# Optimization experiments

Measured on AMD Instinct MI355X. Metric: run time of the kernel, lower is better.

The kernel has to match this reference:

```python
import jax, jax.numpy as jnp
import numpy as np
import math

B, L, D, N = 8, 4096, 1024, 16

def setup_inputs() -> dict:
    key = jax.random.key(0)
    k1, k2, k3, k4, k5, k6 = jax.random.split(key, 6)
    return {
        "x": jax.random.normal(k1, (B, L, D), dtype=jnp.float32),
        "delta": jax.random.normal(k2, (D, N, 1), dtype=jnp.float32),
        "alpha": jax.random.normal(k3, (D, N, 1), dtype=jnp.float32),
        "beta": jax.random.normal(k4, (D, N, 1), dtype=jnp.float32),
        "gamma": jax.random.normal(k5, (D, N), dtype=jnp.float32),
        "omega": jax.random.normal(k6, (D,), dtype=jnp.float32),
    }

def reference(x, delta, alpha, beta, gamma, omega):
    # x: (B, L, D). Unidirectional EMA, no state, no padding mask.
    b, l, d = x.shape
    n_state = gamma.shape[-1]
    scale = math.sqrt(1.0 / n_state)

    residual = x * omega  # (B, L, D)
    xt = jnp.swapaxes(x, -1, -2)  # (B, D, L)

    # EMA coefficients
    p = jax.nn.sigmoid(delta)          # (D, N, 1)
    a = jax.nn.sigmoid(alpha)          # (D, N, 1)
    q = 1.0 - p * a                    # (D, N, 1)

    # Vandermonde kernel: k[d, t] = sum_n p*beta*q^t * gamma*scale
    t = jnp.arange(l, dtype=x.dtype)   # (L,)
    vander = t[None, None, :] * jnp.log(q)          # (D, N, L)
    kernel = p * beta * jnp.exp(vander)             # (D, N, L)
    k = jnp.einsum('dnl,dn->dl', kernel, gamma * scale)  # (D, L)

    # FFT long convolution with zero-padding to 2L (linear conv)
    n_fft = 2 * l
    k_f = jnp.fft.rfft(k, n=n_fft)                  # (D, L+1) complex
    x_f = jnp.fft.rfft(xt, n=n_fft)                 # (B, D, L+1) complex
    out = jnp.fft.irfft(x_f * k_f, n=n_fft)[..., :l]  # (B, D, L)

    return jnp.swapaxes(out, -1, -2) + residual     # (B, L, D)
```

## Files before the change

### kernel.cpp

```cpp
#include <hip/hip_runtime.h>


#define BB 8
#define LL 4096
#define DD 1024
#define NN 16
#define UF 8
#define NB 512

__device__ __forceinline__ float sigmoid_precise(float v) {
    return 1.0f / (1.0f + expf(-v));
}

__device__ __forceinline__ void sc_store(float* p, float v) {
    asm volatile("global_store_dword %0, %1, off sc0 sc1"
                 :: "v"(p), "v"(v) : "memory");
}
__device__ __forceinline__ int sc_load_i(const int* p) {
    int v;
    asm volatile("global_load_dword %0, %1, off sc0 sc1\n\t"
                 "s_waitcnt vmcnt(0)"
                 : "=v"(v) : "v"(p) : "memory");
    return v;
}
__device__ __forceinline__ void sc_load4(const float* p0, const float* p1,
                                         const float* p2, const float* p3,
                                         float& o0, float& o1, float& o2, float& o3) {
    asm volatile(
        "global_load_dword %0, %4, off sc0 sc1\n\t"
        "global_load_dword %1, %5, off sc0 sc1\n\t"
        "global_load_dword %2, %6, off sc0 sc1\n\t"
        "global_load_dword %3, %7, off sc0 sc1\n\t"
        "s_waitcnt vmcnt(0)"
        : "=&v"(o0), "=&v"(o1), "=&v"(o2), "=&v"(o3)
        : "v"(p0), "v"(p1), "v"(p2), "v"(p3)
        : "memory");
}
__device__ __forceinline__ void sc_load8s(const float* p, size_t stride, float* o) {
    const float* a0 = p;
    const float* a1 = p + stride;
    const float* a2 = p + 2 * stride;
    const float* a3 = p + 3 * stride;
    const float* a4 = p + 4 * stride;
    const float* a5 = p + 5 * stride;
    const float* a6 = p + 6 * stride;
    const float* a7 = p + 7 * stride;
    asm volatile(
        "global_load_dword %0, %8, off sc0 sc1\n\t"
        "global_load_dword %1, %9, off sc0 sc1\n\t"
        "global_load_dword %2, %10, off sc0 sc1\n\t"
        "global_load_dword %3, %11, off sc0 sc1\n\t"
        "global_load_dword %4, %12, off sc0 sc1\n\t"
        "global_load_dword %5, %13, off sc0 sc1\n\t"
        "global_load_dword %6, %14, off sc0 sc1\n\t"
        "global_load_dword %7, %15, off sc0 sc1\n\t"
        "s_waitcnt vmcnt(0)"
        : "=&v"(o[0]), "=&v"(o[1]), "=&v"(o[2]), "=&v"(o[3]),
          "=&v"(o[4]), "=&v"(o[5]), "=&v"(o[6]), "=&v"(o[7])
        : "v"(a0), "v"(a1), "v"(a2), "v"(a3),
          "v"(a4), "v"(a5), "v"(a6), "v"(a7)
        : "memory");
}
__device__ __forceinline__ void vm_drain() {
    asm volatile("s_waitcnt vmcnt(0)" ::: "memory");
}

__device__ __forceinline__ void grid_barrier(int* bar) {
    vm_drain();
    __syncthreads();
    if (threadIdx.x == 0) {
        atomicAdd(bar, 1);
        while (sc_load_i(bar) < NB)
            __builtin_amdgcn_s_sleep(2);
    }
    __syncthreads();
}

template <int G_>
__global__ __launch_bounds__(256, 2) void ema_onepass(
    const float* __restrict__ x,
    const float* __restrict__ delta,
    const float* __restrict__ alpha,
    const float* __restrict__ beta,
    const float* __restrict__ gamma,
    const float* __restrict__ omega,
    float* __restrict__ out,
    float* __restrict__ E,
    int*   __restrict__ bar)
{
    constexpr int C_    = LL / G_;
    constexpr int NTASK = (32 * G_) / NB;
    static_assert((C_ & (C_ - 1)) == 0, "C_ must be a power of two");
    static_assert(32 * G_ == NB * NTASK, "task tiling must be exact");

    const int blk   = blockIdx.x;
    const int chain = blk & 31;
    const int b     = chain >> 2;
    const int dblk  = chain & 3;
    const int d     = dblk * 256 + threadIdx.x;

    float q[NN], gc[NN];
#pragma unroll
    for (int n = 0; n < NN; ++n) {
        const float p = sigmoid_precise(delta[d * NN + n]);
        const float a = sigmoid_precise(alpha[d * NN + n]);
        q[n]  = 1.0f - p * a;
        gc[n] = p * beta[d * NN + n] * gamma[d * NN + n] * 0.25f;
    }
    const float om = omega[d];

    for (int k = 0; k < NTASK; ++k) {
        const int g = (blk >> 5) + k * (G_ / NTASK);
        const float* xp = x + ((size_t)b * LL + (size_t)g * C_) * DD + d;

        float u[NN];
#pragma unroll
        for (int n = 0; n < NN; ++n) u[n] = 0.0f;
        for (int ii = 0; ii < C_; ii += UF) {
            float xv[UF];
#pragma unroll
            for (int j = 0; j < UF; ++j)
                xv[j] = xp[(size_t)(ii + j) * DD];
#pragma unroll
            for (int j = 0; j < UF; ++j)
#pragma unroll
                for (int n = 0; n < NN; ++n)
                    u[n] = fmaf(q[n], u[n], xv[j]);
        }
        float* Ep = E + (((size_t)b * G_ + g) * NN) * DD + d;
#pragma unroll
        for (int n = 0; n < NN; ++n)
            sc_store(Ep + (size_t)n * DD, u[n]);
    }

    grid_barrier(&bar[0]);

    {
        const int tt = blk * 256 + threadIdx.x;
        const int sd = tt & (DD - 1);
        const int sn = (tt >> 10) & (NN - 1);
        const int sb = tt >> 14;

        const float sp = sigmoid_precise(delta[sd * NN + sn]);
        const float sa = sigmoid_precise(alpha[sd * NN + sn]);
        const float sq = 1.0f - sp * sa;
        float Qc = sq;
#pragma unroll
        for (int s2 = 1; s2 < C_; s2 <<= 1) Qc *= Qc;

        float* Ep = E + ((size_t)sb * G_ * NN + sn) * DD + sd;
        const size_t gs = (size_t)NN * DD;

        float u = 0.0f;
        for (int gg = 0; gg < G_; gg += UF) {
            float ev[UF];
            sc_load8s(Ep + (size_t)gg * gs, gs, ev);
            float sv[UF];
#pragma unroll
            for (int j = 0; j < UF; ++j) {
                u = fmaf(Qc, u, ev[j]);
                sv[j] = u;
            }
#pragma unroll
            for (int j = 0; j < UF; ++j)
                sc_store(Ep + (size_t)(gg + j) * gs, sv[j]);
        }
    }

    grid_barrier(&bar[1]);

    for (int k = 0; k < NTASK; ++k) {
        const int g = (blk >> 5) + k * (G_ / NTASK);
        const float* xp = x + ((size_t)b * LL + (size_t)g * C_) * DD + d;
        float*       op = out + ((size_t)b * LL + (size_t)g * C_) * DD + d;

        float u[NN];
        if (g > 0) {
            const float* Sp = E + (((size_t)b * G_ + (g - 1)) * NN) * DD + d;
#pragma unroll
            for (int n = 0; n < NN; n += 4)
                sc_load4(Sp + (size_t)(n + 0) * DD, Sp + (size_t)(n + 1) * DD,
                         Sp + (size_t)(n + 2) * DD, Sp + (size_t)(n + 3) * DD,
                         u[n + 0], u[n + 1], u[n + 2], u[n + 3]);
        } else {
#pragma unroll
            for (int n = 0; n < NN; ++n) u[n] = 0.0f;
        }

        for (int ii = 0; ii < C_; ii += UF) {
            float xv[UF];
#pragma unroll
            for (int j = 0; j < UF; ++j)
                xv[j] = xp[(size_t)(ii + j) * DD];
#pragma unroll
            for (int j = 0; j < UF; ++j) {
                const float xvj = xv[j];
                float a0 = om * xvj, a1 = 0.0f, a2 = 0.0f, a3 = 0.0f;
#pragma unroll
                for (int n = 0; n < NN; n += 4) {
                    u[n + 0] = fmaf(q[n + 0], u[n + 0], xvj);
                    u[n + 1] = fmaf(q[n + 1], u[n + 1], xvj);
                    u[n + 2] = fmaf(q[n + 2], u[n + 2], xvj);
                    u[n + 3] = fmaf(q[n + 3], u[n + 3], xvj);
                    a0 = fmaf(gc[n + 0], u[n + 0], a0);
                    a1 = fmaf(gc[n + 1], u[n + 1], a1);
                    a2 = fmaf(gc[n + 2], u[n + 2], a2);
                    a3 = fmaf(gc[n + 3], u[n + 3], a3);
                }
                op[(size_t)(ii + j) * DD] = (a0 + a1) + (a2 + a3);
            }
        }
    }
}

extern "C" void kernel_launch(void* const* d_in, const int* in_sizes, int n_in,
                              void* d_out, int out_size, void* d_ws, size_t ws_size,
                              hipStream_t stream) {
    const float* x     = (const float*)d_in[0];
    const float* delta = (const float*)d_in[1];
    const float* alpha = (const float*)d_in[2];
    const float* beta  = (const float*)d_in[3];
    const float* gamma = (const float*)d_in[4];
    const float* omega = (const float*)d_in[5];
    float* out = (float*)d_out;

    int*   bar = (int*)d_ws;
    float* E   = (float*)((char*)d_ws + 256);

    hipMemsetAsync(d_ws, 0, 256, stream);

    const size_t need64 = 256 + (size_t)BB * 64 * NN * DD * sizeof(float);
    if (ws_size >= need64)
        hipLaunchKernelGGL(ema_onepass<64>, dim3(NB), dim3(256), 0, stream,
                           x, delta, alpha, beta, gamma, omega, out, E, bar);
    else
        hipLaunchKernelGGL(ema_onepass<32>, dim3(NB), dim3(256), 0, stream,
                           x, delta, alpha, beta, gamma, omega, out, E, bar);
}
```

Before: 341.3 us.

## Use one chunk per block with 1024 blocks and double-buffer x loads

Changes the work split so each block handles exactly one chunk: 1024 blocks with G=32 replace 512 blocks with G=64 and two tasks each. Launch bounds move from 2 to 5 blocks per SM so all 1024 blocks can be co-resident for the software grid barrier. Both sequential scan passes now prefetch the next group of x rows while computing the current one, to hide load latency. The larger chunks lengthen each serial scan, and the barrier can deadlock if 1024 blocks do not all fit on the device.

```diff
diff --git a/kernel.cpp b/kernel.cpp
--- a/kernel.cpp
+++ b/kernel.cpp
@@ -6,7 +6,6 @@
 #define DD 1024
 #define NN 16
 #define UF 8
-#define NB 512
 
 __device__ __forceinline__ float sigmoid_precise(float v) {
     return 1.0f / (1.0f + expf(-v));
@@ -65,19 +64,20 @@
     asm volatile("s_waitcnt vmcnt(0)" ::: "memory");
 }
 
+template <int NB_>
 __device__ __forceinline__ void grid_barrier(int* bar) {
     vm_drain();
     __syncthreads();
     if (threadIdx.x == 0) {
         atomicAdd(bar, 1);
-        while (sc_load_i(bar) < NB)
+        while (sc_load_i(bar) < NB_)
             __builtin_amdgcn_s_sleep(2);
     }
     __syncthreads();
 }
 
-template <int G_>
-__global__ __launch_bounds__(256, 2) void ema_onepass(
+template <int G_, int NB_>
+__global__ __launch_bounds__(256, 5) void ema_onepass(
     const float* __restrict__ x,
     const float* __restrict__ delta,
     const float* __restrict__ alpha,
@@ -88,13 +88,13 @@
     float* __restrict__ E,
     int*   __restrict__ bar)
 {
-    constexpr int C_    = LL / G_;
-    constexpr int NTASK = (32 * G_) / NB;
+    constexpr int C_ = LL / G_;
+    static_assert(NB_ == 32 * G_, "one chunk-task per block");
     static_assert((C_ & (C_ - 1)) == 0, "C_ must be a power of two");
-    static_assert(32 * G_ == NB * NTASK, "task tiling must be exact");
 
     const int blk   = blockIdx.x;
     const int chain = blk & 31;
+    const int g     = blk >> 5;
     const int b     = chain >> 2;
     const int dblk  = chain & 3;
     const int d     = dblk * 256 + threadIdx.x;
@@ -109,33 +109,47 @@
     }
     const float om = omega[d];
 
-    for (int k = 0; k < NTASK; ++k) {
-        const int g = (blk >> 5) + k * (G_ / NTASK);
-        const float* xp = x + ((size_t)b * LL + (size_t)g * C_) * DD + d;
-
+    const float* xp = x + ((size_t)b * LL + (size_t)g * C_) * DD + d;
+
+    {
         float u[NN];
 #pragma unroll
         for (int n = 0; n < NN; ++n) u[n] = 0.0f;
-        for (int ii = 0; ii < C_; ii += UF) {
-            float xv[UF];
-#pragma unroll
-            for (int j = 0; j < UF; ++j)
-                xv[j] = xp[(size_t)(ii + j) * DD];
+
+        float xa[UF], xb[UF];
+#pragma unroll
+        for (int j = 0; j < UF; ++j)
+            xa[j] = xp[(size_t)j * DD];
+        for (int ii = 0; ii < C_; ii += 2 * UF) {
+#pragma unroll
+            for (int j = 0; j < UF; ++j)
+                xb[j] = xp[(size_t)(ii + UF + j) * DD];
 #pragma unroll
             for (int j = 0; j < UF; ++j)
 #pragma unroll
                 for (int n = 0; n < NN; ++n)
-                    u[n] = fmaf(q[n], u[n], xv[j]);
-        }
+                    u[n] = fmaf(q[n], u[n], xa[j]);
+            if (ii + 2 * UF < C_) {
+#pragma unroll
+                for (int j = 0; j < UF; ++j)
+                    xa[j] = xp[(size_t)(ii + 2 * UF + j) * DD];
+            }
+#pragma unroll
+            for (int j = 0; j < UF; ++j)
+#pragma unroll
+                for (int n = 0; n < NN; ++n)
+                    u[n] = fmaf(q[n], u[n], xb[j]);
+        }
+
         float* Ep = E + (((size_t)b * G_ + g) * NN) * DD + d;
 #pragma unroll
         for (int n = 0; n < NN; ++n)
             sc_store(Ep + (size_t)n * DD, u[n]);
     }
 
-    grid_barrier(&bar[0]);
-
-    {
+    grid_barrier<NB_>(&bar[0]);
+
+    if (blk * 256 < BB * NN * DD) {
         const int tt = blk * 256 + threadIdx.x;
         const int sd = tt & (DD - 1);
         const int sn = (tt >> 10) & (NN - 1);
@@ -167,13 +181,9 @@
         }
     }
 
-    grid_barrier(&bar[1]);
-
-    for (int k = 0; k < NTASK; ++k) {
-        const int g = (blk >> 5) + k * (G_ / NTASK);
-        const float* xp = x + ((size_t)b * LL + (size_t)g * C_) * DD + d;
-        float*       op = out + ((size_t)b * LL + (size_t)g * C_) * DD + d;
-
+    grid_barrier<NB_>(&bar[1]);
+
+    {
         float u[NN];
         if (g > 0) {
             const float* Sp = E + (((size_t)b * G_ + (g - 1)) * NN) * DD + d;
@@ -187,14 +197,19 @@
             for (int n = 0; n < NN; ++n) u[n] = 0.0f;
         }
 
-        for (int ii = 0; ii < C_; ii += UF) {
-            float xv[UF];
-#pragma unroll
-            for (int j = 0; j < UF; ++j)
-                xv[j] = xp[(size_t)(ii + j) * DD];
+        float* op = out + ((size_t)b * LL + (size_t)g * C_) * DD + d;
+
+        float xa[UF], xb[UF];
+#pragma unroll
+        for (int j = 0; j < UF; ++j)
+            xa[j] = xp[(size_t)j * DD];
+        for (int ii = 0; ii < C_; ii += 2 * UF) {
+#pragma unroll
+            for (int j = 0; j < UF; ++j)
+                xb[j] = xp[(size_t)(ii + UF + j) * DD];
 #pragma unroll
             for (int j = 0; j < UF; ++j) {
-                const float xvj = xv[j];
+                const float xvj = xa[j];
                 float a0 = om * xvj, a1 = 0.0f, a2 = 0.0f, a3 = 0.0f;
 #pragma unroll
                 for (int n = 0; n < NN; n += 4) {
@@ -209,6 +224,28 @@
                 }
                 op[(size_t)(ii + j) * DD] = (a0 + a1) + (a2 + a3);
             }
+            if (ii + 2 * UF < C_) {
+#pragma unroll
+                for (int j = 0; j < UF; ++j)
+                    xa[j] = xp[(size_t)(ii + 2 * UF + j) * DD];
+            }
+#pragma unroll
+            for (int j = 0; j < UF; ++j) {
+                const float xvj = xb[j];
+                float a0 = om * xvj, a1 = 0.0f, a2 = 0.0f, a3 = 0.0f;
+#pragma unroll
+                for (int n = 0; n < NN; n += 4) {
+                    u[n + 0] = fmaf(q[n + 0], u[n + 0], xvj);
+                    u[n + 1] = fmaf(q[n + 1], u[n + 1], xvj);
+                    u[n + 2] = fmaf(q[n + 2], u[n + 2], xvj);
+                    u[n + 3] = fmaf(q[n + 3], u[n + 3], xvj);
+                    a0 = fmaf(gc[n + 0], u[n + 0], a0);
+                    a1 = fmaf(gc[n + 1], u[n + 1], a1);
+                    a2 = fmaf(gc[n + 2], u[n + 2], a2);
+                    a3 = fmaf(gc[n + 3], u[n + 3], a3);
+                }
+                op[(size_t)(ii + UF + j) * DD] = (a0 + a1) + (a2 + a3);
+            }
         }
     }
 }
@@ -229,11 +266,11 @@
 
     hipMemsetAsync(d_ws, 0, 256, stream);
 
-    const size_t need64 = 256 + (size_t)BB * 64 * NN * DD * sizeof(float);
-    if (ws_size >= need64)
-        hipLaunchKernelGGL(ema_onepass<64>, dim3(NB), dim3(256), 0, stream,
-                           x, delta, alpha, beta, gamma, omega, out, E, bar);
+    const size_t need32 = 256 + (size_t)BB * 32 * NN * DD * sizeof(float);
+    if (ws_size >= need32)
+        hipLaunchKernelGGL((ema_onepass<32, 1024>), dim3(1024), dim3(256), 0,
+                           stream, x, delta, alpha, beta, gamma, omega, out, E, bar);
     else
-        hipLaunchKernelGGL(ema_onepass<32>, dim3(NB), dim3(256), 0, stream,
-                           x, delta, alpha, beta, gamma, omega, out, E, bar);
-}
+        hipLaunchKernelGGL((ema_onepass<16, 512>), dim3(512), dim3(256), 0,
+                           stream, x, delta, alpha, beta, gamma, omega, out, E, bar);
+}
```

Result: slower. 403.0 us (+18.1%).

## Interleave two independent chunk recurrences per thread with double-buffered x loads

Applied to the files above, without the earlier changes.

Each thread now processes two chunks (gA and gB = gA + G/2) at once in both the local-scan and output phases. It interleaves their recurrences to expose instruction-level parallelism and double-buffers x register loads so memory latency overlaps the FMA chains. The gc coefficients are computed only after the barrier, which lowers register pressure in the first phase, and carry-in states load through the 8-wide coherent load. The cost is more live registers (two 16-state vectors plus four 8-wide x buffers), which may hurt occupancy under launch_bounds(256,2).

```diff
diff --git a/kernel.cpp b/kernel.cpp
--- a/kernel.cpp
+++ b/kernel.cpp
@@ -22,19 +22,6 @@
                  "s_waitcnt vmcnt(0)"
                  : "=v"(v) : "v"(p) : "memory");
     return v;
-}
-__device__ __forceinline__ void sc_load4(const float* p0, const float* p1,
-                                         const float* p2, const float* p3,
-                                         float& o0, float& o1, float& o2, float& o3) {
-    asm volatile(
-        "global_load_dword %0, %4, off sc0 sc1\n\t"
-        "global_load_dword %1, %5, off sc0 sc1\n\t"
-        "global_load_dword %2, %6, off sc0 sc1\n\t"
-        "global_load_dword %3, %7, off sc0 sc1\n\t"
-        "s_waitcnt vmcnt(0)"
-        : "=&v"(o0), "=&v"(o1), "=&v"(o2), "=&v"(o3)
-        : "v"(p0), "v"(p1), "v"(p2), "v"(p3)
-        : "memory");
 }
 __device__ __forceinline__ void sc_load8s(const float* p, size_t stride, float* o) {
     const float* a0 = p;
@@ -65,12 +52,13 @@
     asm volatile("s_waitcnt vmcnt(0)" ::: "memory");
 }
 
+template <int NB_>
 __device__ __forceinline__ void grid_barrier(int* bar) {
     vm_drain();
     __syncthreads();
     if (threadIdx.x == 0) {
         atomicAdd(bar, 1);
-        while (sc_load_i(bar) < NB)
+        while (sc_load_i(bar) < NB_)
             __builtin_amdgcn_s_sleep(2);
     }
     __syncthreads();
@@ -89,51 +77,85 @@
     int*   __restrict__ bar)
 {
     constexpr int C_    = LL / G_;
-    constexpr int NTASK = (32 * G_) / NB;
+    constexpr int NPAIR = G_ / 32;
+    static_assert(32 * G_ == NB * 2 * NPAIR, "pair tiling must be exact");
     static_assert((C_ & (C_ - 1)) == 0, "C_ must be a power of two");
-    static_assert(32 * G_ == NB * NTASK, "task tiling must be exact");
 
     const int blk   = blockIdx.x;
     const int chain = blk & 31;
+    const int gbase = blk >> 5;
     const int b     = chain >> 2;
     const int dblk  = chain & 3;
     const int d     = dblk * 256 + threadIdx.x;
 
-    float q[NN], gc[NN];
+    float q[NN];
 #pragma unroll
     for (int n = 0; n < NN; ++n) {
         const float p = sigmoid_precise(delta[d * NN + n]);
         const float a = sigmoid_precise(alpha[d * NN + n]);
-        q[n]  = 1.0f - p * a;
-        gc[n] = p * beta[d * NN + n] * gamma[d * NN + n] * 0.25f;
-    }
-    const float om = omega[d];
-
-    for (int k = 0; k < NTASK; ++k) {
-        const int g = (blk >> 5) + k * (G_ / NTASK);
-        const float* xp = x + ((size_t)b * LL + (size_t)g * C_) * DD + d;
-
-        float u[NN];
-#pragma unroll
-        for (int n = 0; n < NN; ++n) u[n] = 0.0f;
-        for (int ii = 0; ii < C_; ii += UF) {
-            float xv[UF];
-#pragma unroll
-            for (int j = 0; j < UF; ++j)
-                xv[j] = xp[(size_t)(ii + j) * DD];
-#pragma unroll
-            for (int j = 0; j < UF; ++j)
-#pragma unroll
-                for (int n = 0; n < NN; ++n)
-                    u[n] = fmaf(q[n], u[n], xv[j]);
-        }
-        float* Ep = E + (((size_t)b * G_ + g) * NN) * DD + d;
-#pragma unroll
-        for (int n = 0; n < NN; ++n)
-            sc_store(Ep + (size_t)n * DD, u[n]);
-    }
-
-    grid_barrier(&bar[0]);
+        q[n] = 1.0f - p * a;
+    }
+
+    for (int p = 0; p < NPAIR; ++p) {
+        const int gA = gbase + p * 16;
+        const int gB = gA + G_ / 2;
+        const float* xA = x + ((size_t)b * LL + (size_t)gA * C_) * DD + d;
+        const float* xB = x + ((size_t)b * LL + (size_t)gB * C_) * DD + d;
+
+        float ua[NN], ub[NN];
+#pragma unroll
+        for (int n = 0; n < NN; ++n) { ua[n] = 0.0f; ub[n] = 0.0f; }
+
+        float a0[UF], b0[UF], a1[UF], b1[UF];
+#pragma unroll
+        for (int j = 0; j < UF; ++j) a0[j] = xA[(size_t)j * DD];
+#pragma unroll
+        for (int j = 0; j < UF; ++j) b0[j] = xB[(size_t)j * DD];
+#pragma unroll
+        for (int j = 0; j < UF; ++j) a1[j] = xA[(size_t)(UF + j) * DD];
+#pragma unroll
+        for (int j = 0; j < UF; ++j) b1[j] = xB[(size_t)(UF + j) * DD];
+
+        for (int ii = 0; ii < C_; ii += 2 * UF) {
+#pragma unroll
+            for (int j = 0; j < UF; ++j)
+#pragma unroll
+                for (int n = 0; n < NN; ++n) ua[n] = fmaf(q[n], ua[n], a0[j]);
+#pragma unroll
+            for (int j = 0; j < UF; ++j)
+#pragma unroll
+                for (int n = 0; n < NN; ++n) ub[n] = fmaf(q[n], ub[n], b0[j]);
+            if (ii + 2 * UF < C_) {
+#pragma unroll
+                for (int j = 0; j < UF; ++j) a0[j] = xA[(size_t)(ii + 2 * UF + j) * DD];
+#pragma unroll
+                for (int j = 0; j < UF; ++j) b0[j] = xB[(size_t)(ii + 2 * UF + j) * DD];
+            }
+#pragma unroll
+            for (int j = 0; j < UF; ++j)
+#pragma unroll
+                for (int n = 0; n < NN; ++n) ua[n] = fmaf(q[n], ua[n], a1[j]);
+#pragma unroll
+            for (int j = 0; j < UF; ++j)
+#pragma unroll
+                for (int n = 0; n < NN; ++n) ub[n] = fmaf(q[n], ub[n], b1[j]);
+            if (ii + 3 * UF < C_) {
+#pragma unroll
+                for (int j = 0; j < UF; ++j) a1[j] = xA[(size_t)(ii + 3 * UF + j) * DD];
+#pragma unroll
+                for (int j = 0; j < UF; ++j) b1[j] = xB[(size_t)(ii + 3 * UF + j) * DD];
+            }
+        }
+
+        float* EpA = E + (((size_t)b * G_ + gA) * NN) * DD + d;
+        float* EpB = E + (((size_t)b * G_ + gB) * NN) * DD + d;
+#pragma unroll
+        for (int n = 0; n < NN; ++n) sc_store(EpA + (size_t)n * DD, ua[n]);
+#pragma unroll
+        for (int n = 0; n < NN; ++n) sc_store(EpB + (size_t)n * DD, ub[n]);
+    }
+
+    grid_barrier<NB>(&bar[0]);
 
     {
         const int tt = blk * 256 + threadIdx.x;
@@ -167,47 +189,129 @@
         }
     }
 
-    grid_barrier(&bar[1]);
-
-    for (int k = 0; k < NTASK; ++k) {
-        const int g = (blk >> 5) + k * (G_ / NTASK);
-        const float* xp = x + ((size_t)b * LL + (size_t)g * C_) * DD + d;
-        float*       op = out + ((size_t)b * LL + (size_t)g * C_) * DD + d;
-
-        float u[NN];
-        if (g > 0) {
-            const float* Sp = E + (((size_t)b * G_ + (g - 1)) * NN) * DD + d;
-#pragma unroll
-            for (int n = 0; n < NN; n += 4)
-                sc_load4(Sp + (size_t)(n + 0) * DD, Sp + (size_t)(n + 1) * DD,
-                         Sp + (size_t)(n + 2) * DD, Sp + (size_t)(n + 3) * DD,
-                         u[n + 0], u[n + 1], u[n + 2], u[n + 3]);
+    grid_barrier<NB>(&bar[1]);
+
+    float gc[NN];
+#pragma unroll
+    for (int n = 0; n < NN; ++n) {
+        const float p = sigmoid_precise(delta[d * NN + n]);
+        gc[n] = p * beta[d * NN + n] * gamma[d * NN + n] * 0.25f;
+    }
+    const float om = omega[d];
+
+    for (int p = 0; p < NPAIR; ++p) {
+        const int gA = gbase + p * 16;
+        const int gB = gA + G_ / 2;
+        const float* xA = x + ((size_t)b * LL + (size_t)gA * C_) * DD + d;
+        const float* xB = x + ((size_t)b * LL + (size_t)gB * C_) * DD + d;
+        float* oA = out + ((size_t)b * LL + (size_t)gA * C_) * DD + d;
+        float* oB = out + ((size_t)b * LL + (size_t)gB * C_) * DD + d;
+
+        float ua[NN], ub[NN];
+        if (gA > 0) {
+            const float* Sp = E + (((size_t)b * G_ + (gA - 1)) * NN) * DD + d;
+            sc_load8s(Sp, (size_t)DD, ua);
+            sc_load8s(Sp + (size_t)8 * DD, (size_t)DD, ua + 8);
         } else {
 #pragma unroll
-            for (int n = 0; n < NN; ++n) u[n] = 0.0f;
-        }
-
-        for (int ii = 0; ii < C_; ii += UF) {
-            float xv[UF];
-#pragma unroll
-            for (int j = 0; j < UF; ++j)
-                xv[j] = xp[(size_t)(ii + j) * DD];
-#pragma unroll
-            for (int j = 0; j < UF; ++j) {
-                const float xvj = xv[j];
-                float a0 = om * xvj, a1 = 0.0f, a2 = 0.0f, a3 = 0.0f;
+            for (int n = 0; n < NN; ++n) ua[n] = 0.0f;
+        }
+        {
+            const float* Sp = E + (((size_t)b * G_ + (gB - 1)) * NN) * DD + d;
+            sc_load8s(Sp, (size_t)DD, ub);
+            sc_load8s(Sp + (size_t)8 * DD, (size_t)DD, ub + 8);
+        }
+
+        float a0[UF], b0[UF], a1[UF], b1[UF];
+#pragma unroll
+        for (int j = 0; j < UF; ++j) a0[j] = xA[(size_t)j * DD];
+#pragma unroll
+        for (int j = 0; j < UF; ++j) b0[j] = xB[(size_t)j * DD];
+#pragma unroll
+        for (int j = 0; j < UF; ++j) a1[j] = xA[(size_t)(UF + j) * DD];
+#pragma unroll
+        for (int j = 0; j < UF; ++j) b1[j] = xB[(size_t)(UF + j) * DD];
+
+        for (int ii = 0; ii < C_; ii += 2 * UF) {
+#pragma unroll
+            for (int j = 0; j < UF; ++j) {
+                const float xv = a0[j];
+                float s0 = om * xv, s1 = 0.0f, s2 = 0.0f, s3 = 0.0f;
 #pragma unroll
                 for (int n = 0; n < NN; n += 4) {
-                    u[n + 0] = fmaf(q[n + 0], u[n + 0], xvj);
-                    u[n + 1] = fmaf(q[n + 1], u[n + 1], xvj);
-                    u[n + 2] = fmaf(q[n + 2], u[n + 2], xvj);
-                    u[n + 3] = fmaf(q[n + 3], u[n + 3], xvj);
-                    a0 = fmaf(gc[n + 0], u[n + 0], a0);
-                    a1 = fmaf(gc[n + 1], u[n + 1], a1);
-                    a2 = fmaf(gc[n + 2], u[n + 2], a2);
-                    a3 = fmaf(gc[n + 3], u[n + 3], a3);
+                    ua[n + 0] = fmaf(q[n + 0], ua[n + 0], xv);
+                    ua[n + 1] = fmaf(q[n + 1], ua[n + 1], xv);
+                    ua[n + 2] = fmaf(q[n + 2], ua[n + 2], xv);
+                    ua[n + 3] = fmaf(q[n + 3], ua[n + 3], xv);
+                    s0 = fmaf(gc[n + 0], ua[n + 0], s0);
+                    s1 = fmaf(gc[n + 1], ua[n + 1], s1);
+                    s2 = fmaf(gc[n + 2], ua[n + 2], s2);
+                    s3 = fmaf(gc[n + 3], ua[n + 3], s3);
                 }
-                op[(size_t)(ii + j) * DD] = (a0 + a1) + (a2 + a3);
+                oA[(size_t)(ii + j) * DD] = (s0 + s1) + (s2 + s3);
+            }
+#pragma unroll
+            for (int j = 0; j < UF; ++j) {
+                const float xv = b0[j];
+                float s0 = om * xv, s1 = 0.0f, s2 = 0.0f, s3 = 0.0f;
+#pragma unroll
+                for (int n = 0; n < NN; n += 4) {
+                    ub[n + 0] = fmaf(q[n + 0], ub[n + 0], xv);
+                    ub[n + 1] = fmaf(q[n + 1], ub[n + 1], xv);
+                    ub[n + 2] = fmaf(q[n + 2], ub[n + 2], xv);
+                    ub[n + 3] = fmaf(q[n + 3], ub[n + 3], xv);
+                    s0 = fmaf(gc[n + 0], ub[n + 0], s0);
+                    s1 = fmaf(gc[n + 1], ub[n + 1], s1);
+                    s2 = fmaf(gc[n + 2], ub[n + 2], s2);
+                    s3 = fmaf(gc[n + 3], ub[n + 3], s3);
+                }
+                oB[(size_t)(ii + j) * DD] = (s0 + s1) + (s2 + s3);
+            }
+            if (ii + 2 * UF < C_) {
+#pragma unroll
+                for (int j = 0; j < UF; ++j) a0[j] = xA[(size_t)(ii + 2 * UF + j) * DD];
+#pragma unroll
+                for (int j = 0; j < UF; ++j) b0[j] = xB[(size_t)(ii + 2 * UF + j) * DD];
+            }
+#pragma unroll
+            for (int j = 0; j < UF; ++j) {
+                const float xv = a1[j];
+                float s0 = om * xv, s1 = 0.0f, s2 = 0.0f, s3 = 0.0f;
+#pragma unroll
+                for (int n = 0; n < NN; n += 4) {
+                    ua[n + 0] = fmaf(q[n + 0], ua[n + 0], xv);
+                    ua[n + 1] = fmaf(q[n + 1], ua[n + 1], xv);
+                    ua[n + 2] = fmaf(q[n + 2], ua[n + 2], xv);
+                    ua[n + 3] = fmaf(q[n + 3], ua[n + 3], xv);
+                    s0 = fmaf(gc[n + 0], ua[n + 0], s0);
+                    s1 = fmaf(gc[n + 1], ua[n + 1], s1);
+                    s2 = fmaf(gc[n + 2], ua[n + 2], s2);
+                    s3 = fmaf(gc[n + 3], ua[n + 3], s3);
+                }
+                oA[(size_t)(ii + UF + j) * DD] = (s0 + s1) + (s2 + s3);
+            }
+#pragma unroll
+            for (int j = 0; j < UF; ++j) {
+                const float xv = b1[j];
+                float s0 = om * xv, s1 = 0.0f, s2 = 0.0f, s3 = 0.0f;
+#pragma unroll
+                for (int n = 0; n < NN; n += 4) {
+                    ub[n + 0] = fmaf(q[n + 0], ub[n + 0], xv);
+                    ub[n + 1] = fmaf(q[n + 1], ub[n + 1], xv);
+                    ub[n + 2] = fmaf(q[n + 2], ub[n + 2], xv);
+                    ub[n + 3] = fmaf(q[n + 3], ub[n + 3], xv);
+                    s0 = fmaf(gc[n + 0], ub[n + 0], s0);
+                    s1 = fmaf(gc[n + 1], ub[n + 1], s1);
+                    s2 = fmaf(gc[n + 2], ub[n + 2], s2);
+                    s3 = fmaf(gc[n + 3], ub[n + 3], s3);
+                }
+                oB[(size_t)(ii + UF + j) * DD] = (s0 + s1) + (s2 + s3);
+            }
+            if (ii + 3 * UF < C_) {
+#pragma unroll
+                for (int j = 0; j < UF; ++j) a1[j] = xA[(size_t)(ii + 3 * UF + j) * DD];
+#pragma unroll
+                for (int j = 0; j < UF; ++j) b1[j] = xB[(size_t)(ii + 3 * UF + j) * DD];
             }
         }
     }
```

After: 348.4 us. 1.02x slower.
